# Optimization experiments

Measured on AMD Instinct MI355X. Metric: run time of the kernel, lower is better.

## Reference

```python
import jax, jax.numpy as jnp
import numpy as np

B = 16          # batch (num decode sequences)
H = 16          # num heads (== num kv heads)
D = 128         # head dim
BLOCK = 16      # tokens per cache block
BPS = 128       # blocks per sequence
NB = B * BPS    # total cache blocks = 2048
S = BPS * BLOCK # max context len per seq = 2048
SCALE = 0.08838834764831845  # 1/sqrt(128)


def setup_inputs() -> dict:
    key = jax.random.key(0)
    ks = jax.random.split(key, 5)
    q = jax.random.normal(ks[0], (B, H, D), dtype=jnp.float32)
    k = jax.random.normal(ks[1], (B, H, D), dtype=jnp.float32)
    v = jax.random.normal(ks[2], (B, H, D), dtype=jnp.float32)
    k_cache = jax.random.normal(ks[3], (NB, BLOCK, H, D), dtype=jnp.float32)
    v_cache = jax.random.normal(ks[4], (NB, BLOCK, H, D), dtype=jnp.float32)
    # identity paged layout: seq i owns blocks [i*BPS, (i+1)*BPS)
    block_tables = jnp.arange(NB, dtype=jnp.int32).reshape(B, BPS)
    # new token goes into the last slot of each sequence's last block
    slot_mapping = (jnp.arange(B, dtype=jnp.int32) * BPS + (BPS - 1)) * BLOCK + (BLOCK - 1)
    context_lens = jnp.full((B,), S, dtype=jnp.int32)
    return {"q": q, "k": k, "v": v, "k_cache": k_cache, "v_cache": v_cache,
            "block_tables": block_tables, "slot_mapping": slot_mapping,
            "context_lens": context_lens}


def reference(q, k, v, k_cache, v_cache, block_tables, slot_mapping, context_lens):
    nb, block_size, h, d = k_cache.shape
    b = q.shape[0]
    # --- store_kvcache: scatter new K/V token into flat cache (all slots valid) ---
    flat_k = k_cache.reshape(nb * block_size, h, d).at[slot_mapping].set(k)
    flat_v = v_cache.reshape(nb * block_size, h, d).at[slot_mapping].set(v)
    kc = flat_k.reshape(nb, block_size, h, d)
    vc = flat_v.reshape(nb, block_size, h, d)
    # --- paged gather: [B, BPS, BLOCK, H, D] -> [B, S, H, D] ---
    k_seq = kc[block_tables].reshape(b, -1, h, d)
    v_seq = vc[block_tables].reshape(b, -1, h, d)
    s = k_seq.shape[1]
    # --- masked single-token attention (q_len = 1) ---
    scores = jnp.einsum('bhd,bshd->bhs', q, k_seq) * SCALE
    mask = jnp.arange(s, dtype=jnp.int32)[None, :] < context_lens[:, None]  # [B, S]
    scores = jnp.where(mask[:, None, :], scores, -jnp.inf)
    p = jax.nn.softmax(scores, axis=-1)
    o = jnp.einsum('bhs,bshd->bhd', p, v_seq)  # [B, H, D]
    return o
```

## Files before the change

kernel.cpp:

```cpp
#include <hip/hip_runtime.h>
#include <math.h>

#define BB   16
#define HH   16
#define DD   128
#define BLK  16
#define BPS  128
#define SS   2048
#define SCALE_F 0.08838834764831845f

#define NTHREADS 1024
#define NWAVES   16
#define TPW      (SS/NWAVES)

__global__ __launch_bounds__(NTHREADS, 1)
void paged_decode(const float* __restrict__ q,
                  const float* __restrict__ knew,
                  const float* __restrict__ vnew,
                  const float* __restrict__ kc,
                  const float* __restrict__ vc,
                  const int*   __restrict__ bt,
                  const int*   __restrict__ smap_g,
                  const int*   __restrict__ clen,
                  float*       __restrict__ out)
{
    __shared__ float sc[SS];
    __shared__ int   rb[SS];
    __shared__ float part[NWAVES][DD];
    __shared__ int   smap[BB];
    __shared__ float red[NWAVES];
    __shared__ float bmax, bsum;

    const int bid  = blockIdx.x;
    const int b    = bid >> 4;
    const int h    = bid & 15;
    const int t    = threadIdx.x;
    const int lane = t & 63;
    const int wave = t >> 6;
    const int len  = clen[b];

    if (t < BB) smap[t] = smap_g[t];
    __syncthreads();

    for (int s = t; s < SS; s += NTHREADS) {
        int pb   = bt[b * BPS + (s >> 4)];
        int slot = pb * BLK + (s & 15);
        int enc  = (slot * HH + h) * DD;
        #pragma unroll
        for (int j = 0; j < BB; ++j)
            if (slot == smap[j]) enc = -(j + 1);
        rb[s] = enc;
    }
    __syncthreads();

    const int half = lane >> 5;
    const int d4   = lane & 31;
    const float4 q4 = *(const float4*)(q + (b * HH + h) * DD + d4 * 4);
    const int s0 = wave * TPW;

    #pragma unroll 4
    for (int i = 0; i < TPW / 2; ++i) {
        int s   = s0 + i * 2 + half;
        int enc = rb[s];
        const float* kp = (enc >= 0)
            ? (kc + enc + d4 * 4)
            : (knew + ((-enc - 1) * HH + h) * DD + d4 * 4);
        float4 kv = *(const float4*)kp;
        float dot = q4.x * kv.x + q4.y * kv.y + q4.z * kv.z + q4.w * kv.w;
        dot += __shfl_xor(dot, 1);
        dot += __shfl_xor(dot, 2);
        dot += __shfl_xor(dot, 4);
        dot += __shfl_xor(dot, 8);
        dot += __shfl_xor(dot, 16);
        if (d4 == 0) sc[s] = (s < len) ? dot * SCALE_F : -1e30f;
    }
    __syncthreads();

    float m = fmaxf(sc[t], sc[t + NTHREADS]);
    #pragma unroll
    for (int msk = 32; msk >= 1; msk >>= 1)
        m = fmaxf(m, __shfl_xor(m, msk));
    if (lane == 0) red[wave] = m;
    __syncthreads();
    if (wave == 0) {
        float v = (lane < NWAVES) ? red[lane] : -1e30f;
        #pragma unroll
        for (int msk = 8; msk >= 1; msk >>= 1)
            v = fmaxf(v, __shfl_xor(v, msk));
        if (lane == 0) bmax = v;
    }
    __syncthreads();

    const float M = bmax;
    float e0 = expf(sc[t] - M);
    float e1 = expf(sc[t + NTHREADS] - M);
    sc[t] = e0;
    sc[t + NTHREADS] = e1;
    float sum = e0 + e1;
    #pragma unroll
    for (int msk = 32; msk >= 1; msk >>= 1)
        sum += __shfl_xor(sum, msk);
    if (lane == 0) red[wave] = sum;
    __syncthreads();
    if (wave == 0) {
        float v = (lane < NWAVES) ? red[lane] : 0.f;
        #pragma unroll
        for (int msk = 8; msk >= 1; msk >>= 1)
            v += __shfl_xor(v, msk);
        if (lane == 0) bsum = v;
    }
    __syncthreads();

    float4 acc = make_float4(0.f, 0.f, 0.f, 0.f);
    #pragma unroll 4
    for (int i = 0; i < TPW / 2; ++i) {
        int s   = s0 + i * 2 + half;
        float p = sc[s];
        int enc = rb[s];
        const float* vp = (enc >= 0)
            ? (vc + enc + d4 * 4)
            : (vnew + ((-enc - 1) * HH + h) * DD + d4 * 4);
        float4 vv = *(const float4*)vp;
        acc.x += p * vv.x;
        acc.y += p * vv.y;
        acc.z += p * vv.z;
        acc.w += p * vv.w;
    }
    acc.x += __shfl_xor(acc.x, 32);
    acc.y += __shfl_xor(acc.y, 32);
    acc.z += __shfl_xor(acc.z, 32);
    acc.w += __shfl_xor(acc.w, 32);
    if (lane < 32) *(float4*)&part[wave][d4 * 4] = acc;
    __syncthreads();

    if (t < DD) {
        float o = 0.f;
        #pragma unroll
        for (int w = 0; w < NWAVES; ++w) o += part[w][t];
        out[(b * HH + h) * DD + t] = o / bsum;
    }
}

extern "C" void kernel_launch(void* const* d_in, const int* in_sizes, int n_in,
                              void* d_out, int out_size, void* d_ws, size_t ws_size,
                              hipStream_t stream)
{
    const float* q    = (const float*)d_in[0];
    const float* knew = (const float*)d_in[1];
    const float* vnew = (const float*)d_in[2];
    const float* kc   = (const float*)d_in[3];
    const float* vc   = (const float*)d_in[4];
    const int*   bt   = (const int*)d_in[5];
    const int*   smap = (const int*)d_in[6];
    const int*   clen = (const int*)d_in[7];
    float*       out  = (float*)d_out;

    paged_decode<<<dim3(BB * HH), dim3(NTHREADS), 0, stream>>>(
        q, knew, vnew, kc, vc, bt, smap, clen, out);
}
```

Before: 105.8 us.

## Split context across blocks with flash-decoding partials and a combine kernel

Replaces the single 1024-thread block per (batch, head) with 8 smaller 256-thread blocks, each handling a 256-token chunk. Each block writes its local max, local sum and unnormalized output to workspace, and a second kernel rescales and merges them. The goal is more independent blocks across the CUs and less intra-block synchronization, so the memory-bound KV streaming gets more parallelism. The cost is an extra kernel launch and a small workspace round trip.

Result: faster. 98.84 us (-6.6%).

```diff
diff --git a/kernel.cpp b/kernel.cpp
--- a/kernel.cpp
+++ b/kernel.cpp
@@ -9,59 +9,66 @@
 #define SS   2048
 #define SCALE_F 0.08838834764831845f
 
-#define NTHREADS 1024
-#define NWAVES   16
-#define TPW      (SS/NWAVES)
+#define SPLIT 8
+#define CHUNK (SS / SPLIT)
+#define NT1   256
+#define NW1   4
+#define TPW1  (CHUNK / NW1)
 
-__global__ __launch_bounds__(NTHREADS, 1)
-void paged_decode(const float* __restrict__ q,
-                  const float* __restrict__ knew,
-                  const float* __restrict__ vnew,
-                  const float* __restrict__ kc,
-                  const float* __restrict__ vc,
-                  const int*   __restrict__ bt,
-                  const int*   __restrict__ smap_g,
-                  const int*   __restrict__ clen,
-                  float*       __restrict__ out)
+__global__ __launch_bounds__(NT1, 8)
+void pd_partial(const float* __restrict__ q,
+                const float* __restrict__ knew,
+                const float* __restrict__ vnew,
+                const float* __restrict__ kc,
+                const float* __restrict__ vc,
+                const int*   __restrict__ bt,
+                const int*   __restrict__ smap_g,
+                const int*   __restrict__ clen,
+                float*       __restrict__ ml,
+                float*       __restrict__ pacc)
 {
-    __shared__ float sc[SS];
-    __shared__ int   rb[SS];
-    __shared__ float part[NWAVES][DD];
+    __shared__ float sc[CHUNK];
+    __shared__ int   rb[CHUNK];
+    __shared__ float part[NW1][DD];
     __shared__ int   smap[BB];
-    __shared__ float red[NWAVES];
-    __shared__ float bmax, bsum;
+    __shared__ float redm[NW1], reds[NW1];
 
     const int bid  = blockIdx.x;
-    const int b    = bid >> 4;
-    const int h    = bid & 15;
+    const int c    = bid & (SPLIT - 1);
+    const int bh   = bid >> 3;
+    const int b    = bh >> 4;
+    const int h    = bh & 15;
     const int t    = threadIdx.x;
     const int lane = t & 63;
     const int wave = t >> 6;
     const int len  = clen[b];
+    const int sbase = c * CHUNK;
 
     if (t < BB) smap[t] = smap_g[t];
     __syncthreads();
 
-    for (int s = t; s < SS; s += NTHREADS) {
+    {
+        int s    = sbase + t;
         int pb   = bt[b * BPS + (s >> 4)];
         int slot = pb * BLK + (s & 15);
         int enc  = (slot * HH + h) * DD;
         #pragma unroll
         for (int j = 0; j < BB; ++j)
             if (slot == smap[j]) enc = -(j + 1);
-        rb[s] = enc;
+        rb[t] = enc;
     }
     __syncthreads();
 
     const int half = lane >> 5;
     const int d4   = lane & 31;
-    const float4 q4 = *(const float4*)(q + (b * HH + h) * DD + d4 * 4);
-    const int s0 = wave * TPW;
+    const float4 q4 = *(const float4*)(q + bh * DD + d4 * 4);
+    const int w0 = wave * TPW1;
 
-    #pragma unroll 4
-    for (int i = 0; i < TPW / 2; ++i) {
-        int s   = s0 + i * 2 + half;
-        int enc = rb[s];
+    #pragma unroll 8
+    for (int i = 0; i < TPW1 / 2; ++i) {
+        int sl  = w0 + i * 2 + half;
+        int s   = sbase + sl;
+        int enc = rb[sl];
         const float* kp = (enc >= 0)
             ? (kc + enc + d4 * 4)
             : (knew + ((-enc - 1) * HH + h) * DD + d4 * 4);
@@ -72,51 +79,33 @@
         dot += __shfl_xor(dot, 4);
         dot += __shfl_xor(dot, 8);
         dot += __shfl_xor(dot, 16);
-        if (d4 == 0) sc[s] = (s < len) ? dot * SCALE_F : -1e30f;
+        if (d4 == 0) sc[sl] = (s < len) ? dot * SCALE_F : -1e30f;
     }
     __syncthreads();
 
-    float m = fmaxf(sc[t], sc[t + NTHREADS]);
+    float m = sc[t];
     #pragma unroll
     for (int msk = 32; msk >= 1; msk >>= 1)
         m = fmaxf(m, __shfl_xor(m, msk));
-    if (lane == 0) red[wave] = m;
+    if (lane == 0) redm[wave] = m;
     __syncthreads();
-    if (wave == 0) {
-        float v = (lane < NWAVES) ? red[lane] : -1e30f;
-        #pragma unroll
-        for (int msk = 8; msk >= 1; msk >>= 1)
-            v = fmaxf(v, __shfl_xor(v, msk));
-        if (lane == 0) bmax = v;
-    }
-    __syncthreads();
+    const float M = fmaxf(fmaxf(redm[0], redm[1]), fmaxf(redm[2], redm[3]));
 
-    const float M = bmax;
-    float e0 = expf(sc[t] - M);
-    float e1 = expf(sc[t + NTHREADS] - M);
-    sc[t] = e0;
-    sc[t + NTHREADS] = e1;
-    float sum = e0 + e1;
+    float e = expf(sc[t] - M);
+    sc[t] = e;
+    float ssum = e;
     #pragma unroll
     for (int msk = 32; msk >= 1; msk >>= 1)
-        sum += __shfl_xor(sum, msk);
-    if (lane == 0) red[wave] = sum;
-    __syncthreads();
-    if (wave == 0) {
-        float v = (lane < NWAVES) ? red[lane] : 0.f;
-        #pragma unroll
-        for (int msk = 8; msk >= 1; msk >>= 1)
-            v += __shfl_xor(v, msk);
-        if (lane == 0) bsum = v;
-    }
+        ssum += __shfl_xor(ssum, msk);
+    if (lane == 0) reds[wave] = ssum;
     __syncthreads();
 
     float4 acc = make_float4(0.f, 0.f, 0.f, 0.f);
-    #pragma unroll 4
-    for (int i = 0; i < TPW / 2; ++i) {
-        int s   = s0 + i * 2 + half;
-        float p = sc[s];
-        int enc = rb[s];
+    #pragma unroll 8
+    for (int i = 0; i < TPW1 / 2; ++i) {
+        int sl  = w0 + i * 2 + half;
+        float p = sc[sl];
+        int enc = rb[sl];
         const float* vp = (enc >= 0)
             ? (vc + enc + d4 * 4)
             : (vnew + ((-enc - 1) * HH + h) * DD + d4 * 4);
@@ -134,11 +123,40 @@
     __syncthreads();
 
     if (t < DD) {
-        float o = 0.f;
-        #pragma unroll
-        for (int w = 0; w < NWAVES; ++w) o += part[w][t];
-        out[(b * HH + h) * DD + t] = o / bsum;
+        float o = part[0][t] + part[1][t] + part[2][t] + part[3][t];
+        pacc[bid * DD + t] = o;
     }
+    if (t == 0) {
+        float L = reds[0] + reds[1] + reds[2] + reds[3];
+        ml[bid * 2]     = M;
+        ml[bid * 2 + 1] = L;
+    }
+}
+
+__global__ __launch_bounds__(DD)
+void pd_combine(const float* __restrict__ ml,
+                const float* __restrict__ pacc,
+                float*       __restrict__ out)
+{
+    const int bh = blockIdx.x;
+    const int t  = threadIdx.x;
+
+    float m[SPLIT], l[SPLIT];
+    float M = -1e30f;
+    #pragma unroll
+    for (int i = 0; i < SPLIT; ++i) {
+        m[i] = ml[(bh * SPLIT + i) * 2];
+        l[i] = ml[(bh * SPLIT + i) * 2 + 1];
+        M = fmaxf(M, m[i]);
+    }
+    float denom = 0.f, o = 0.f;
+    #pragma unroll
+    for (int i = 0; i < SPLIT; ++i) {
+        float w = expf(m[i] - M);
+        denom += w * l[i];
+        o     += w * pacc[(bh * SPLIT + i) * DD + t];
+    }
+    out[bh * DD + t] = o / denom;
 }
 
 extern "C" void kernel_launch(void* const* d_in, const int* in_sizes, int n_in,
@@ -155,6 +173,10 @@
     const int*   clen = (const int*)d_in[7];
     float*       out  = (float*)d_out;
 
-    paged_decode<<<dim3(BB * HH), dim3(NTHREADS), 0, stream>>>(
-        q, knew, vnew, kc, vc, bt, smap, clen, out);
+    float* ml   = (float*)d_ws;
+    float* pacc = (float*)d_ws + BB * HH * SPLIT * 2;
+
+    pd_partial<<<dim3(BB * HH * SPLIT), dim3(NT1), 0, stream>>>(
+        q, knew, vnew, kc, vc, bt, smap, clen, ml, pacc);
+    pd_combine<<<dim3(BB * HH), dim3(DD), 0, stream>>>(ml, pacc, out);
 }
```
